# Kernel tuning notes

Hardware: AMD Instinct MI355X
Metric: run time of the kernel (lower is better)

The kernel has to match this reference:

```python
import jax, jax.numpy as jnp
import numpy as np

N_NODES = 50000
N_EDGES = 800000
IN_DIM = 128
HID = 64
NUM_GRAPHS = 64


def _gcn_conv(x, W, b, src, dst, num_nodes):
    """PyG GCNConv: out = D^-1/2 (A+I) D^-1/2 (x W) + b, messages scattered to dst."""
    h = x @ W  # [N, out]
    ones = jnp.ones((src.shape[0],), dtype=x.dtype)
    # degree at target nodes, self-loop adds 1
    deg = jax.ops.segment_sum(ones, dst, num_segments=num_nodes) + 1.0
    dinv = jax.lax.rsqrt(deg)  # [N]
    norm = dinv[src] * dinv[dst]  # [E]
    msgs = h[src] * norm[:, None]  # [E, out] gather-scale
    agg = jax.ops.segment_sum(msgs, dst, num_segments=num_nodes)  # scatter-add
    # self-loop contribution: norm_ii = dinv[i]^2
    agg = agg + h * (dinv * dinv)[:, None]
    return agg + b


def setup_inputs() -> dict:
    key = jax.random.key(0)
    k = jax.random.split(key, 10)
    x = jax.random.normal(k[0], (N_NODES, IN_DIM), dtype=jnp.float32)
    edge_index = jax.random.randint(k[1], (2, N_EDGES), 0, N_NODES, dtype=jnp.int32)
    batch = jnp.sort(jax.random.randint(k[2], (N_NODES,), 0, NUM_GRAPHS, dtype=jnp.int32))
    # Glorot-ish params
    W1 = jax.random.normal(k[3], (IN_DIM, HID), dtype=jnp.float32) / np.sqrt(IN_DIM)
    b1 = jnp.zeros((HID,), dtype=jnp.float32)
    W2 = jax.random.normal(k[4], (HID, HID), dtype=jnp.float32) / np.sqrt(HID)
    b2 = jnp.zeros((HID,), dtype=jnp.float32)
    Wlin = jax.random.normal(k[5], (HID, 1), dtype=jnp.float32) / np.sqrt(HID)
    blin = jnp.zeros((1,), dtype=jnp.float32)
    return {"x": x, "edge_index": edge_index, "batch": batch,
            "W1": W1, "b1": b1, "W2": W2, "b2": b2, "Wlin": Wlin, "blin": blin}


def reference(x, edge_index, batch, W1, b1, W2, b2, Wlin, blin):
    src, dst = edge_index[0], edge_index[1]
    h = _gcn_conv(x, W1, b1, src, dst, N_NODES)
    h = jax.nn.relu(h)  # dropout is identity in eval mode
    h = _gcn_conv(h, W2, b2, src, dst, N_NODES)
    h = jax.nn.relu(h)
    # global mean pool per graph
    sums = jax.ops.segment_sum(h, batch, num_segments=NUM_GRAPHS)  # [G, HID]
    cnts = jax.ops.segment_sum(jnp.ones((N_NODES,), h.dtype), batch, num_segments=NUM_GRAPHS)
    pooled = sums / jnp.maximum(cnts, 1.0)[:, None]
    return pooled @ Wlin + blin  # [G, 1]
```

## Files before the change

kernel.cpp:

```cpp
#include <hip/hip_runtime.h>
#include <hip/hip_fp16.h>

#define N_NODES 50000
#define N_EDGES 800000
#define IN_DIM 128
#define HID 64
#define NUM_GRAPHS 64
#define NB 196
#define NBLK 64

__device__ inline float4 load_h4(const __half* p) {
    const __half2* q = (const __half2*)p;
    float2 a = __half22float2(q[0]);
    float2 b = __half22float2(q[1]);
    return make_float4(a.x, a.y, b.x, b.y);
}
__device__ inline void store_h4(__half* p, float4 v) {
    __half2* q = (__half2*)p;
    q[0] = __floats2half2_rn(v.x, v.y);
    q[1] = __floats2half2_rn(v.z, v.w);
}
__device__ inline void load_h8(const __half* p, float* f) {
    float4 r = *(const float4*)p;
    const __half2* h = (const __half2*)&r;
    float2 a0 = __half22float2(h[0]);
    float2 a1 = __half22float2(h[1]);
    float2 a2 = __half22float2(h[2]);
    float2 a3 = __half22float2(h[3]);
    f[0] = a0.x; f[1] = a0.y; f[2] = a1.x; f[3] = a1.y;
    f[4] = a2.x; f[5] = a2.y; f[6] = a3.x; f[7] = a3.y;
}
__device__ inline void store_h8(__half* p, const float* f) {
    __half2 hs[4];
    hs[0] = __floats2half2_rn(f[0], f[1]);
    hs[1] = __floats2half2_rn(f[2], f[3]);
    hs[2] = __floats2half2_rn(f[4], f[5]);
    hs[3] = __floats2half2_rn(f[6], f[7]);
    *(float4*)p = *(const float4*)hs;
}

template <int K, typename TIN, bool SCALE>
__device__ __forceinline__ void gemm_body(const TIN* __restrict__ A, const float* __restrict__ W,
                                          const float* __restrict__ dinv, __half* __restrict__ out,
                                          int nRows, int node0, float* xs, float* ws) {
    int tid = threadIdx.x;
    int c0 = (tid & 15) * 4, n0 = (tid >> 4) * 4;
    float acc[4][4] = {};
    for (int kb = 0; kb < K; kb += 64) {
        for (int i = tid; i < 64 * 16; i += 256) {
            int k = i >> 4, c4 = (i & 15) * 4;
            *(float4*)&ws[k * 68 + c4] = *(const float4*)&W[(size_t)(kb + k) * 64 + c4];
        }
        for (int i = tid; i < 64 * 16; i += 256) {
            int n = i >> 4, k4 = (i & 15) * 4;
            int gn = node0 + n;
            float4 v;
            if (gn < nRows) {
                if constexpr (sizeof(TIN) == 4) v = *(const float4*)&A[(size_t)gn * K + kb + k4];
                else                            v = load_h4((const __half*)&A[(size_t)gn * K + kb + k4]);
            } else v = make_float4(0.f, 0.f, 0.f, 0.f);
            *(float4*)&xs[n * 68 + k4] = v;
        }
        __syncthreads();
        for (int k = 0; k < 64; k += 4) {
            float4 x0 = *(const float4*)&xs[(n0 + 0) * 68 + k];
            float4 x1 = *(const float4*)&xs[(n0 + 1) * 68 + k];
            float4 x2 = *(const float4*)&xs[(n0 + 2) * 68 + k];
            float4 x3 = *(const float4*)&xs[(n0 + 3) * 68 + k];
            #define KSTEP(KK, F) { \
                float4 wr = *(const float4*)&ws[(k + KK) * 68 + c0]; \
                acc[0][0] += x0.F * wr.x; acc[0][1] += x0.F * wr.y; acc[0][2] += x0.F * wr.z; acc[0][3] += x0.F * wr.w; \
                acc[1][0] += x1.F * wr.x; acc[1][1] += x1.F * wr.y; acc[1][2] += x1.F * wr.z; acc[1][3] += x1.F * wr.w; \
                acc[2][0] += x2.F * wr.x; acc[2][1] += x2.F * wr.y; acc[2][2] += x2.F * wr.z; acc[2][3] += x2.F * wr.w; \
                acc[3][0] += x3.F * wr.x; acc[3][1] += x3.F * wr.y; acc[3][2] += x3.F * wr.z; acc[3][3] += x3.F * wr.w; }
            KSTEP(0, x)
            KSTEP(1, y)
            KSTEP(2, z)
            KSTEP(3, w)
            #undef KSTEP
        }
        __syncthreads();
    }
    #pragma unroll
    for (int i = 0; i < 4; i++) {
        int gn = node0 + n0 + i;
        if (gn < nRows) {
            float sc = 1.0f;
            if constexpr (SCALE) sc = dinv[gn];
            store_h4(&out[(size_t)gn * 64 + c0],
                     make_float4(acc[i][0] * sc, acc[i][1] * sc, acc[i][2] * sc, acc[i][3] * sc));
        }
    }
}

__global__ __launch_bounds__(256) void k1_kernel(const int* __restrict__ dst, int* __restrict__ hist_g,
                                                 const float* __restrict__ x, const float* __restrict__ W1,
                                                 __half* __restrict__ h1) {
    __shared__ __align__(16) float smem[2 * 64 * 68];
    int blk = blockIdx.x, tid = threadIdx.x;
    if (blk < NBLK) {
        int* h = (int*)smem;
        for (int i = tid; i < NB; i += 256) h[i] = 0;
        __syncthreads();
        const int NI = N_EDGES / 4;
        for (int i = blk * 256 + tid; i < NI; i += NBLK * 256) {
            int4 d = ((const int4*)dst)[i];
            atomicAdd(&h[d.x >> 8], 1);
            atomicAdd(&h[d.y >> 8], 1);
            atomicAdd(&h[d.z >> 8], 1);
            atomicAdd(&h[d.w >> 8], 1);
        }
        __syncthreads();
        for (int i = tid; i < NB; i += 256) hist_g[i * NBLK + blk] = h[i];
    } else {
        int node0 = (blk - NBLK) * 64;
        gemm_body<IN_DIM, float, false>(x, W1, nullptr, h1, N_NODES, node0, smem, smem + 64 * 68);
    }
}

__global__ __launch_bounds__(256) void k2_binscan(const int* __restrict__ hist_g,
                                                  const int* __restrict__ src, const int* __restrict__ dst,
                                                  int* __restrict__ binned, int* __restrict__ bstart,
                                                  int* __restrict__ offs) {
    __shared__ int ld[NB * NBLK];
    __shared__ int cur[NB];
    __shared__ int wsum[4];
    int tid = threadIdx.x, blk = blockIdx.x;
    for (int i = tid; i < NB * NBLK; i += 256) ld[i] = hist_g[i];
    __syncthreads();
    const int CH = (NB * NBLK) / 256;
    int base = tid * CH;
    int s = 0;
    for (int k = 0; k < CH; k++) { int v = ld[base + k]; ld[base + k] = s; s += v; }
    int lane = tid & 63, wid = tid >> 6;
    int inc = s;
    #pragma unroll
    for (int d = 1; d < 64; d <<= 1) { int t = __shfl_up(inc, d, 64); if (lane >= d) inc += t; }
    if (lane == 63) wsum[wid] = inc;
    __syncthreads();
    if (tid == 0) {
        int a = 0;
        for (int w = 0; w < 4; w++) { int t = wsum[w]; wsum[w] = a; a += t; }
    }
    __syncthreads();
    int off = wsum[wid] + inc - s;
    for (int k = 0; k < CH; k++) ld[base + k] += off;
    __syncthreads();
    for (int b = tid; b < NB; b += 256) cur[b] = ld[b * NBLK + blk];
    if (blk == 0) {
        for (int b = tid; b < NB; b += 256) bstart[b] = ld[b * NBLK];
        if (tid == 0) { bstart[NB] = N_EDGES; offs[N_NODES] = N_EDGES; }
    }
    __syncthreads();
    const int NI = N_EDGES / 4;
    for (int i = blk * 256 + tid; i < NI; i += NBLK * 256) {
        int4 sv = ((const int4*)src)[i];
        int4 dv = ((const int4*)dst)[i];
        int p0 = atomicAdd(&cur[dv.x >> 8], 1); binned[p0] = (sv.x & 0xFFFF) | ((dv.x & 255) << 16);
        int p1 = atomicAdd(&cur[dv.y >> 8], 1); binned[p1] = (sv.y & 0xFFFF) | ((dv.y & 255) << 16);
        int p2 = atomicAdd(&cur[dv.z >> 8], 1); binned[p2] = (sv.z & 0xFFFF) | ((dv.z & 255) << 16);
        int p3 = atomicAdd(&cur[dv.w >> 8], 1); binned[p3] = (sv.w & 0xFFFF) | ((dv.w & 255) << 16);
    }
}

__global__ __launch_bounds__(256) void build_kernel(const int* __restrict__ binned, const int* __restrict__ bstart,
                                                    int* __restrict__ offs, float* __restrict__ dinv,
                                                    unsigned short* __restrict__ csr_src) {
    __shared__ int cnt[256];
    __shared__ int excl[256];
    __shared__ int rnk[256];
    __shared__ int wtot[4];
    int b = blockIdx.x, tid = threadIdx.x;
    int base = bstart[b];
    int end  = bstart[b + 1];
    cnt[tid] = 0; rnk[tid] = 0;
    __syncthreads();
    for (int j = base + tid; j < end; j += 256) atomicAdd(&cnt[(binned[j] >> 16) & 255], 1);
    __syncthreads();
    int v = cnt[tid];
    int lane = tid & 63, wid = tid >> 6;
    int inc = v;
    #pragma unroll
    for (int d = 1; d < 64; d <<= 1) { int t = __shfl_up(inc, d, 64); if (lane >= d) inc += t; }
    if (lane == 63) wtot[wid] = inc;
    __syncthreads();
    if (tid == 0) {
        int a = 0;
        for (int w = 0; w < 4; w++) { int t = wtot[w]; wtot[w] = a; a += t; }
    }
    __syncthreads();
    excl[tid] = wtot[wid] + inc - v;
    int node = b * 256 + tid;
    if (node < N_NODES) {
        offs[node] = base + excl[tid];
        dinv[node] = rsqrtf((float)v + 1.0f);
    }
    __syncthreads();
    for (int j = base + tid; j < end; j += 256) {
        int e = binned[j];
        int l = (e >> 16) & 255;
        int r = atomicAdd(&rnk[l], 1);
        csr_src[base + excl[l] + r] = (unsigned short)(e & 0xFFFF);
    }
}

__global__ __launch_bounds__(256) void agg1_kernel(const __half* __restrict__ hd, const int* __restrict__ offs,
                                                   const unsigned short* __restrict__ csr_src,
                                                   const float* __restrict__ dinv, const float* __restrict__ bias,
                                                   __half* __restrict__ out) {
    int lane = threadIdx.x & 63;
    int node = blockIdx.x * 4 + (threadIdx.x >> 6);
    int g = lane >> 3;
    int cc = (lane & 7) * 8;
    float acc[8] = {};
    int beg = offs[node], end = offs[node + 1];
    #pragma unroll 2
    for (int j = beg + g; j < end; j += 8) {
        int s = csr_src[j];
        float dv = dinv[s];
        float hv[8];
        load_h8(&hd[(size_t)s * 64 + cc], hv);
        #pragma unroll
        for (int i = 0; i < 8; i++) acc[i] = fmaf(hv[i], dv, acc[i]);
    }
    #pragma unroll
    for (int m = 8; m <= 32; m <<= 1) {
        #pragma unroll
        for (int i = 0; i < 8; i++) acc[i] += __shfl_xor(acc[i], m, 64);
    }
    if (g == 0) {
        float di = dinv[node];
        float d2 = di * di;
        float hn[8];
        load_h8(&hd[(size_t)node * 64 + cc], hn);
        float4 bv0 = *(const float4*)&bias[cc];
        float4 bv1 = *(const float4*)&bias[cc + 4];
        float bb[8] = {bv0.x, bv0.y, bv0.z, bv0.w, bv1.x, bv1.y, bv1.z, bv1.w};
        float r[8];
        #pragma unroll
        for (int i = 0; i < 8; i++) r[i] = fmaxf(fmaf(di, acc[i], fmaf(d2, hn[i], bb[i])), 0.0f);
        store_h8(&out[(size_t)node * 64 + cc], r);
    }
}

__global__ __launch_bounds__(256) void gemm2_kernel(const __half* __restrict__ A, const float* __restrict__ W,
                                                    const float* __restrict__ dinv, __half* __restrict__ out) {
    __shared__ __align__(16) float smem[2 * 64 * 68];
    gemm_body<HID, __half, true>(A, W, dinv, out, N_NODES, blockIdx.x * 64, smem, smem + 64 * 68);
}

__global__ __launch_bounds__(256) void agg2dot_kernel(const __half* __restrict__ hd, const int* __restrict__ offs,
                                                      const unsigned short* __restrict__ csr_src,
                                                      const float* __restrict__ dinv, const float* __restrict__ bias,
                                                      const float* __restrict__ Wlin,
                                                      float* __restrict__ ndot) {
    int lane = threadIdx.x & 63;
    int node = blockIdx.x * 4 + (threadIdx.x >> 6);
    int g = lane >> 3;
    int cc = (lane & 7) * 8;
    float acc[8] = {};
    int beg = offs[node], end = offs[node + 1];
    #pragma unroll 2
    for (int j = beg + g; j < end; j += 8) {
        int s = csr_src[j];
        float hv[8];
        load_h8(&hd[(size_t)s * 64 + cc], hv);
        #pragma unroll
        for (int i = 0; i < 8; i++) acc[i] += hv[i];
    }
    #pragma unroll
    for (int m = 8; m <= 32; m <<= 1) {
        #pragma unroll
        for (int i = 0; i < 8; i++) acc[i] += __shfl_xor(acc[i], m, 64);
    }
    if (g == 0) {
        float di = dinv[node];
        float hn[8];
        load_h8(&hd[(size_t)node * 64 + cc], hn);
        float4 bv0 = *(const float4*)&bias[cc];
        float4 bv1 = *(const float4*)&bias[cc + 4];
        float bb[8] = {bv0.x, bv0.y, bv0.z, bv0.w, bv1.x, bv1.y, bv1.z, bv1.w};
        float4 wl0 = *(const float4*)&Wlin[cc];
        float4 wl1 = *(const float4*)&Wlin[cc + 4];
        float ww[8] = {wl0.x, wl0.y, wl0.z, wl0.w, wl1.x, wl1.y, wl1.z, wl1.w};
        float d = 0.0f;
        #pragma unroll
        for (int i = 0; i < 8; i++) {
            float r = fmaxf(fmaf(di, acc[i] + hn[i], bb[i]), 0.0f);
            d = fmaf(r, ww[i], d);
        }
        #pragma unroll
        for (int m = 1; m < 8; m <<= 1) d += __shfl_xor(d, m, 64);
        if ((lane & 7) == 0) ndot[node] = d;
    }
}

__global__ __launch_bounds__(256) void graphred_kernel(const float* __restrict__ ndot, const int* __restrict__ batch,
                                                       const float* __restrict__ blin, float* __restrict__ out) {
    __shared__ float wpart[4];
    int g = blockIdx.x;
    int tid = threadIdx.x;
    int lo = 0, hi = N_NODES;
    while (lo < hi) { int m = (lo + hi) >> 1; if (batch[m] < g) lo = m + 1; else hi = m; }
    int lo2 = lo, hi2 = N_NODES;
    while (lo2 < hi2) { int m = (lo2 + hi2) >> 1; if (batch[m] < g + 1) lo2 = m + 1; else hi2 = m; }
    float s = 0.0f;
    for (int i = lo + tid; i < lo2; i += 256) s += ndot[i];
    int lane = tid & 63, wid = tid >> 6;
    #pragma unroll
    for (int m = 32; m > 0; m >>= 1) s += __shfl_down(s, m, 64);
    if (lane == 0) wpart[wid] = s;
    __syncthreads();
    if (tid == 0) {
        float t = wpart[0] + wpart[1] + wpart[2] + wpart[3];
        float cnt = (float)(lo2 - lo);
        out[g] = t / fmaxf(cnt, 1.0f) + blin[0];
    }
}

extern "C" void kernel_launch(void* const* d_in, const int* in_sizes, int n_in,
                              void* d_out, int out_size, void* d_ws, size_t ws_size,
                              hipStream_t stream) {
    const float* x    = (const float*)d_in[0];
    const int*   ei   = (const int*)d_in[1];
    const int*   batch= (const int*)d_in[2];
    const float* W1   = (const float*)d_in[3];
    const float* b1   = (const float*)d_in[4];
    const float* W2   = (const float*)d_in[5];
    const float* b2   = (const float*)d_in[6];
    const float* Wlin = (const float*)d_in[7];
    const float* blin = (const float*)d_in[8];
    float* out = (float*)d_out;
    const int* srcA = ei;
    const int* dstA = ei + N_EDGES;

    char* p = (char*)d_ws;
    auto alloc = [&](size_t n) { char* r = p; p += (n + 255) & ~(size_t)255; return r; };
    int*    hist_g  = (int*)alloc((size_t)NB * NBLK * 4);
    int*    bstart  = (int*)alloc((size_t)(NB + 1) * 4);
    int*    offs    = (int*)alloc((size_t)(N_NODES + 1) * 4);
    int*    binned  = (int*)alloc((size_t)N_EDGES * 4);
    unsigned short* csr_src = (unsigned short*)alloc((size_t)N_EDGES * 2);
    float*  dinv    = (float*)alloc((size_t)N_NODES * 4);
    float*  ndot    = (float*)alloc((size_t)N_NODES * 4);
    __half* bufA    = (__half*)alloc((size_t)N_NODES * 64 * 2);
    __half* bufB    = (__half*)alloc((size_t)N_NODES * 64 * 2);

    const int GEMM1_BLOCKS = (N_NODES + 63) / 64;
    k1_kernel<<<NBLK + GEMM1_BLOCKS, 256, 0, stream>>>(dstA, hist_g, x, W1, bufA);
    k2_binscan<<<NBLK, 256, 0, stream>>>(hist_g, srcA, dstA, binned, bstart, offs);
    build_kernel<<<NB, 256, 0, stream>>>(binned, bstart, offs, dinv, csr_src);
    agg1_kernel<<<N_NODES / 4, 256, 0, stream>>>(bufA, offs, csr_src, dinv, b1, bufB);
    gemm2_kernel<<<GEMM1_BLOCKS, 256, 0, stream>>>(bufB, W2, dinv, bufA);
    agg2dot_kernel<<<N_NODES / 4, 256, 0, stream>>>(bufA, offs, csr_src, dinv, b2, Wlin, ndot);
    graphred_kernel<<<NUM_GRAPHS, 256, 0, stream>>>(ndot, batch, blin, out);
}
```

Baseline: 196.6 us.

## Replace two-level binned CSR build with global-atomic degree count, scan, scatter

```diff
diff --git a/kernel.cpp b/kernel.cpp
--- a/kernel.cpp
+++ b/kernel.cpp
@@ -6,8 +6,8 @@
 #define IN_DIM 128
 #define HID 64
 #define NUM_GRAPHS 64
-#define NB 196
 #define NBLK 64
+#define SCAN_BLOCKS 196
 
 __device__ inline float4 load_h4(const __half* p) {
     const __half2* q = (const __half2*)p;
@@ -93,114 +93,71 @@
     }
 }
 
-__global__ __launch_bounds__(256) void k1_kernel(const int* __restrict__ dst, int* __restrict__ hist_g,
+__global__ __launch_bounds__(256) void k1_kernel(const int* __restrict__ dst, int* __restrict__ deg,
                                                  const float* __restrict__ x, const float* __restrict__ W1,
                                                  __half* __restrict__ h1) {
     __shared__ __align__(16) float smem[2 * 64 * 68];
     int blk = blockIdx.x, tid = threadIdx.x;
     if (blk < NBLK) {
-        int* h = (int*)smem;
-        for (int i = tid; i < NB; i += 256) h[i] = 0;
-        __syncthreads();
         const int NI = N_EDGES / 4;
         for (int i = blk * 256 + tid; i < NI; i += NBLK * 256) {
             int4 d = ((const int4*)dst)[i];
-            atomicAdd(&h[d.x >> 8], 1);
-            atomicAdd(&h[d.y >> 8], 1);
-            atomicAdd(&h[d.z >> 8], 1);
-            atomicAdd(&h[d.w >> 8], 1);
-        }
-        __syncthreads();
-        for (int i = tid; i < NB; i += 256) hist_g[i * NBLK + blk] = h[i];
+            atomicAdd(&deg[d.x], 1);
+            atomicAdd(&deg[d.y], 1);
+            atomicAdd(&deg[d.z], 1);
+            atomicAdd(&deg[d.w], 1);
+        }
     } else {
         int node0 = (blk - NBLK) * 64;
         gemm_body<IN_DIM, float, false>(x, W1, nullptr, h1, N_NODES, node0, smem, smem + 64 * 68);
     }
 }
 
-__global__ __launch_bounds__(256) void k2_binscan(const int* __restrict__ hist_g,
-                                                  const int* __restrict__ src, const int* __restrict__ dst,
-                                                  int* __restrict__ binned, int* __restrict__ bstart,
-                                                  int* __restrict__ offs) {
-    __shared__ int ld[NB * NBLK];
-    __shared__ int cur[NB];
-    __shared__ int wsum[4];
-    int tid = threadIdx.x, blk = blockIdx.x;
-    for (int i = tid; i < NB * NBLK; i += 256) ld[i] = hist_g[i];
+__global__ __launch_bounds__(256) void scan_kernel(const int* __restrict__ deg, int* __restrict__ offs,
+                                                   int* __restrict__ cur, float* __restrict__ dinv) {
+    __shared__ int wsA[4];
+    __shared__ int wsB[4];
+    int b = blockIdx.x, tid = threadIdx.x;
+    int lane = tid & 63, wid = tid >> 6;
+    int lo = b * 256;
+    const int4* d4 = (const int4*)deg;
+    int sum = 0;
+    for (int i = tid; i < (lo >> 2); i += 256) { int4 v = d4[i]; sum += v.x + v.y + v.z + v.w; }
+    int r = sum;
+    #pragma unroll
+    for (int m = 1; m < 64; m <<= 1) r += __shfl_xor(r, m, 64);
+    if (lane == 0) wsA[wid] = r;
     __syncthreads();
-    const int CH = (NB * NBLK) / 256;
-    int base = tid * CH;
-    int s = 0;
-    for (int k = 0; k < CH; k++) { int v = ld[base + k]; ld[base + k] = s; s += v; }
-    int lane = tid & 63, wid = tid >> 6;
-    int inc = s;
+    int pre = wsA[0] + wsA[1] + wsA[2] + wsA[3];
+    int node = lo + tid;
+    int v = (node < N_NODES) ? deg[node] : 0;
+    int inc = v;
     #pragma unroll
     for (int d = 1; d < 64; d <<= 1) { int t = __shfl_up(inc, d, 64); if (lane >= d) inc += t; }
-    if (lane == 63) wsum[wid] = inc;
+    if (lane == 63) wsB[wid] = inc;
     __syncthreads();
-    if (tid == 0) {
-        int a = 0;
-        for (int w = 0; w < 4; w++) { int t = wsum[w]; wsum[w] = a; a += t; }
-    }
+    if (tid == 0) { int a = 0; for (int w = 0; w < 4; w++) { int t = wsB[w]; wsB[w] = a; a += t; } }
     __syncthreads();
-    int off = wsum[wid] + inc - s;
-    for (int k = 0; k < CH; k++) ld[base + k] += off;
-    __syncthreads();
-    for (int b = tid; b < NB; b += 256) cur[b] = ld[b * NBLK + blk];
-    if (blk == 0) {
-        for (int b = tid; b < NB; b += 256) bstart[b] = ld[b * NBLK];
-        if (tid == 0) { bstart[NB] = N_EDGES; offs[N_NODES] = N_EDGES; }
-    }
-    __syncthreads();
+    int excl = pre + wsB[wid] + inc - v;
+    if (node < N_NODES) {
+        offs[node] = excl;
+        cur[node]  = excl;
+        dinv[node] = rsqrtf((float)v + 1.0f);
+    }
+    if (b == SCAN_BLOCKS - 1 && tid == 0) offs[N_NODES] = N_EDGES;
+}
+
+__global__ __launch_bounds__(256) void scatter_kernel(const int* __restrict__ src, const int* __restrict__ dst,
+                                                      int* __restrict__ cur, unsigned short* __restrict__ csr_src) {
     const int NI = N_EDGES / 4;
-    for (int i = blk * 256 + tid; i < NI; i += NBLK * 256) {
-        int4 sv = ((const int4*)src)[i];
-        int4 dv = ((const int4*)dst)[i];
-        int p0 = atomicAdd(&cur[dv.x >> 8], 1); binned[p0] = (sv.x & 0xFFFF) | ((dv.x & 255) << 16);
-        int p1 = atomicAdd(&cur[dv.y >> 8], 1); binned[p1] = (sv.y & 0xFFFF) | ((dv.y & 255) << 16);
-        int p2 = atomicAdd(&cur[dv.z >> 8], 1); binned[p2] = (sv.z & 0xFFFF) | ((dv.z & 255) << 16);
-        int p3 = atomicAdd(&cur[dv.w >> 8], 1); binned[p3] = (sv.w & 0xFFFF) | ((dv.w & 255) << 16);
-    }
-}
-
-__global__ __launch_bounds__(256) void build_kernel(const int* __restrict__ binned, const int* __restrict__ bstart,
-                                                    int* __restrict__ offs, float* __restrict__ dinv,
-                                                    unsigned short* __restrict__ csr_src) {
-    __shared__ int cnt[256];
-    __shared__ int excl[256];
-    __shared__ int rnk[256];
-    __shared__ int wtot[4];
-    int b = blockIdx.x, tid = threadIdx.x;
-    int base = bstart[b];
-    int end  = bstart[b + 1];
-    cnt[tid] = 0; rnk[tid] = 0;
-    __syncthreads();
-    for (int j = base + tid; j < end; j += 256) atomicAdd(&cnt[(binned[j] >> 16) & 255], 1);
-    __syncthreads();
-    int v = cnt[tid];
-    int lane = tid & 63, wid = tid >> 6;
-    int inc = v;
-    #pragma unroll
-    for (int d = 1; d < 64; d <<= 1) { int t = __shfl_up(inc, d, 64); if (lane >= d) inc += t; }
-    if (lane == 63) wtot[wid] = inc;
-    __syncthreads();
-    if (tid == 0) {
-        int a = 0;
-        for (int w = 0; w < 4; w++) { int t = wtot[w]; wtot[w] = a; a += t; }
-    }
-    __syncthreads();
-    excl[tid] = wtot[wid] + inc - v;
-    int node = b * 256 + tid;
-    if (node < N_NODES) {
-        offs[node] = base + excl[tid];
-        dinv[node] = rsqrtf((float)v + 1.0f);
-    }
-    __syncthreads();
-    for (int j = base + tid; j < end; j += 256) {
-        int e = binned[j];
-        int l = (e >> 16) & 255;
-        int r = atomicAdd(&rnk[l], 1);
-        csr_src[base + excl[l] + r] = (unsigned short)(e & 0xFFFF);
+    int stride = gridDim.x * 256;
+    for (int i = blockIdx.x * 256 + threadIdx.x; i < NI; i += stride) {
+        int4 s = ((const int4*)src)[i];
+        int4 d = ((const int4*)dst)[i];
+        int p0 = atomicAdd(&cur[d.x], 1); csr_src[p0] = (unsigned short)s.x;
+        int p1 = atomicAdd(&cur[d.y], 1); csr_src[p1] = (unsigned short)s.y;
+        int p2 = atomicAdd(&cur[d.z], 1); csr_src[p2] = (unsigned short)s.z;
+        int p3 = atomicAdd(&cur[d.w], 1); csr_src[p3] = (unsigned short)s.w;
     }
 }
 
@@ -336,20 +293,21 @@
 
     char* p = (char*)d_ws;
     auto alloc = [&](size_t n) { char* r = p; p += (n + 255) & ~(size_t)255; return r; };
-    int*    hist_g  = (int*)alloc((size_t)NB * NBLK * 4);
-    int*    bstart  = (int*)alloc((size_t)(NB + 1) * 4);
+    int*    deg     = (int*)alloc((size_t)N_NODES * 4);
+    int*    cur     = (int*)alloc((size_t)N_NODES * 4);
     int*    offs    = (int*)alloc((size_t)(N_NODES + 1) * 4);
-    int*    binned  = (int*)alloc((size_t)N_EDGES * 4);
     unsigned short* csr_src = (unsigned short*)alloc((size_t)N_EDGES * 2);
     float*  dinv    = (float*)alloc((size_t)N_NODES * 4);
     float*  ndot    = (float*)alloc((size_t)N_NODES * 4);
     __half* bufA    = (__half*)alloc((size_t)N_NODES * 64 * 2);
     __half* bufB    = (__half*)alloc((size_t)N_NODES * 64 * 2);
 
+    hipMemsetAsync(deg, 0, (size_t)N_NODES * 4, stream);
+
     const int GEMM1_BLOCKS = (N_NODES + 63) / 64;
-    k1_kernel<<<NBLK + GEMM1_BLOCKS, 256, 0, stream>>>(dstA, hist_g, x, W1, bufA);
-    k2_binscan<<<NBLK, 256, 0, stream>>>(hist_g, srcA, dstA, binned, bstart, offs);
-    build_kernel<<<NB, 256, 0, stream>>>(binned, bstart, offs, dinv, csr_src);
+    k1_kernel<<<NBLK + GEMM1_BLOCKS, 256, 0, stream>>>(dstA, deg, x, W1, bufA);
+    scan_kernel<<<SCAN_BLOCKS, 256, 0, stream>>>(deg, offs, cur, dinv);
+    scatter_kernel<<<256, 256, 0, stream>>>(srcA, dstA, cur, csr_src);
     agg1_kernel<<<N_NODES / 4, 256, 0, stream>>>(bufA, offs, csr_src, dinv, b1, bufB);
     gemm2_kernel<<<GEMM1_BLOCKS, 256, 0, stream>>>(bufB, W2, dinv, bufA);
     agg2dot_kernel<<<N_NODES / 4, 256, 0, stream>>>(bufA, offs, csr_src, dinv, b2, Wlin, ndot);
```

New measurement: 247.2 us. 25.7% more time.
